# Kernel optimization log

Hardware: AMD Instinct MI355X
Metric: run time of the kernel (lower is better)

## Reference

```python
import jax, jax.numpy as jnp
import numpy as np


def setup_inputs() -> dict:
    key = jax.random.key(0)
    k1, k2, k3, k4, k5, k6 = jax.random.split(key, 6)
    B, S, V, E, H = 64, 128, 50257, 1024, 1024
    scale_ih = 1.0 / np.sqrt(H)
    return {
        "question_tokens": jax.random.randint(k1, (B, S), 0, V, dtype=jnp.int64),
        "emb_weights": jax.random.normal(k2, (V, E), dtype=jnp.float32),
        "w_ih": jax.random.normal(k3, (3 * H, E), dtype=jnp.float32) * scale_ih,
        "w_hh": jax.random.normal(k4, (3 * H, H), dtype=jnp.float32) * scale_ih,
        "b_ih": jax.random.normal(k5, (3 * H,), dtype=jnp.float32) * scale_ih,
        "b_hh": jax.random.normal(k6, (3 * H,), dtype=jnp.float32) * scale_ih,
    }


def _gru_last_hidden(tokens, emb_weights, w_ih, w_hh, b_ih, b_hh):
    # tokens: [B, S]; torch module transposes to seq-first, equivalent here.
    H = w_hh.shape[1]
    x = emb_weights[tokens]                                  # [B, S, E]
    # Precompute input projections for all timesteps (hoisted out of recurrence).
    x_proj = jnp.einsum("bse,ge->sbg", x, w_ih) + b_ih      # [S, B, 3H]

    def step(h, xp):
        # PyTorch GRU gate order: r, z, n
        hp = h @ w_hh.T + b_hh                               # [B, 3H]
        xr, xz, xn = xp[:, :H], xp[:, H:2 * H], xp[:, 2 * H:]
        hr, hz, hn = hp[:, :H], hp[:, H:2 * H], hp[:, 2 * H:]
        r = jax.nn.sigmoid(xr + hr)
        z = jax.nn.sigmoid(xz + hz)
        n = jnp.tanh(xn + r * hn)
        h_new = (1.0 - z) * n + z * h
        return h_new, None

    h0 = jnp.zeros((tokens.shape[0], H), dtype=emb_weights.dtype)
    hT, _ = jax.lax.scan(step, h0, x_proj)
    return hT                                                # [B, H]


def reference(question_tokens, emb_weights, w_ih, w_hh, b_ih, b_hh):
    return _gru_last_hidden(question_tokens, emb_weights, w_ih, w_hh, b_ih, b_hh)
```

## Files before the change

kernel.cpp:

```cpp
#include <hip/hip_runtime.h>
#include <hip/hip_bf16.h>
#include <math.h>

#define GRU_B 64
#define GRU_S 128
#define GRU_E 1024
#define GRU_H 1024
#define GRU_G 3072

typedef _Float16 half8 __attribute__((ext_vector_type(8)));
typedef _Float16 half4v __attribute__((ext_vector_type(4)));
typedef float floatx4 __attribute__((ext_vector_type(4)));

__device__ __forceinline__ half8 cvt_h8(float4 a, float4 b) {
    half8 r;
    r[0] = (_Float16)a.x; r[1] = (_Float16)a.y;
    r[2] = (_Float16)a.z; r[3] = (_Float16)a.w;
    r[4] = (_Float16)b.x; r[5] = (_Float16)b.y;
    r[6] = (_Float16)b.z; r[7] = (_Float16)b.w;
    return r;
}

__global__ __launch_bounds__(256) void xproj_mfma(
    const int* __restrict__ tokens,
    const float* __restrict__ emb,
    const float* __restrict__ w_ih,
    const float* __restrict__ b_ih,
    _Float16* __restrict__ xproj)
{
    __shared__ __attribute__((aligned(16))) _Float16 Al[128 * 32];
    __shared__ __attribute__((aligned(16))) _Float16 Bl[128 * 32];
    __shared__ int toks[128];

    const int t  = threadIdx.x;
    const int m0 = blockIdx.x * 128;
    const int n0 = blockIdx.y * 128;

    if (t < 128) {
        int m = m0 + t;
        toks[t] = tokens[(m & 63) * GRU_S + (m >> 6)];
    }

    const int wid = t >> 6;
    const int l   = t & 63;
    const int wm  = (wid >> 1) * 64;
    const int wn  = (wid & 1) * 64;

    const int sr   = t >> 1;
    const int skw  = (sr >> 1) & 3;
    const int gb   = (t & 1) * 2;

    const int fr   = l & 15;
    const int ag   = l >> 4;
    const int skey = (fr >> 1) & 3;
    const int gfr  = (ag ^ skey) * 16;

    char* ab = reinterpret_cast<char*>(Al);
    char* bb = reinterpret_cast<char*>(Bl);

    floatx4 acc[4][4];
#pragma unroll
    for (int i = 0; i < 4; ++i)
#pragma unroll
        for (int j = 0; j < 4; ++j)
            acc[i][j] = (floatx4){0.f, 0.f, 0.f, 0.f};

    for (int k0 = 0; k0 < GRU_E; k0 += 32) {
        __syncthreads();
        {
            const float4* asrc = reinterpret_cast<const float4*>(
                emb + (size_t)toks[sr] * GRU_E + k0 + (t & 1) * 16);
            const float4* bsrc = reinterpret_cast<const float4*>(
                w_ih + (size_t)(n0 + sr) * GRU_E + k0 + (t & 1) * 16);
            float4 a0 = asrc[0], a1 = asrc[1], a2 = asrc[2], a3 = asrc[3];
            float4 b0 = bsrc[0], b1 = bsrc[1], b2 = bsrc[2], b3 = bsrc[3];
            *reinterpret_cast<half8*>(ab + sr * 64 + ((gb + 0) ^ skw) * 16) = cvt_h8(a0, a1);
            *reinterpret_cast<half8*>(ab + sr * 64 + ((gb + 1) ^ skw) * 16) = cvt_h8(a2, a3);
            *reinterpret_cast<half8*>(bb + sr * 64 + ((gb + 0) ^ skw) * 16) = cvt_h8(b0, b1);
            *reinterpret_cast<half8*>(bb + sr * 64 + ((gb + 1) ^ skw) * 16) = cvt_h8(b2, b3);
        }
        __syncthreads();

        half8 a4[4], b4[4];
#pragma unroll
        for (int mi = 0; mi < 4; ++mi)
            a4[mi] = *reinterpret_cast<const half8*>(ab + (wm + mi * 16 + fr) * 64 + gfr);
#pragma unroll
        for (int ni = 0; ni < 4; ++ni)
            b4[ni] = *reinterpret_cast<const half8*>(bb + (wn + ni * 16 + fr) * 64 + gfr);
#pragma unroll
        for (int mi = 0; mi < 4; ++mi)
#pragma unroll
            for (int ni = 0; ni < 4; ++ni)
                acc[mi][ni] = __builtin_amdgcn_mfma_f32_16x16x32_f16(
                    a4[mi], b4[ni], acc[mi][ni], 0, 0, 0);
    }

    const int cr = (l >> 4) * 4;
    const int cc = l & 15;
#pragma unroll
    for (int ni = 0; ni < 4; ++ni) {
        int n = n0 + wn + ni * 16 + cc;
        float bias = b_ih[n];
#pragma unroll
        for (int mi = 0; mi < 4; ++mi) {
#pragma unroll
            for (int q = 0; q < 4; ++q) {
                int m = m0 + wm + mi * 16 + cr + q;
                xproj[(size_t)m * GRU_G + n] = (_Float16)(acc[mi][ni][q] + bias);
            }
        }
    }
}

__global__ __launch_bounds__(256) void gru_persist(
    const _Float16* __restrict__ xproj,
    const float* __restrict__ w_hh,
    const float* __restrict__ b_hh,
    _Float16* __restrict__ ring,
    float* __restrict__ out,
    int* __restrict__ flags)
{
    __shared__ __attribute__((aligned(16))) _Float16 wlds[48 * 1024];

    __builtin_amdgcn_fence(__ATOMIC_ACQUIRE, "agent");

    const int t   = threadIdx.x;
    const int jb  = blockIdx.x;
    const int l   = t & 63;
    const int wid = t >> 6;
    const int m0  = wid * 16;

    const size_t BUFE = (size_t)GRU_B * GRU_H;
    const size_t BUFQ = BUFE / 4;

    {
        char* wbp = reinterpret_cast<char*>(wlds);
        for (int r = 0; r < 48; ++r) {
            int grow = (r >> 4) * GRU_H + jb * 16 + (r & 15);
            float4 v = reinterpret_cast<const float4*>(
                w_hh + (size_t)grow * GRU_H)[t];
            half4v hv;
            hv.x = (_Float16)v.x; hv.y = (_Float16)v.y;
            hv.z = (_Float16)v.z; hv.w = (_Float16)v.w;
            int g = (t >> 1) ^ (r & 7);
            *reinterpret_cast<half4v*>(wbp + r * 2048 + g * 16 + (t & 1) * 8) = hv;
        }
    }

    {
        unsigned long long* z =
            reinterpret_cast<unsigned long long*>(ring) + 127 * BUFQ;
        int i0 = jb * 256 + t;
        (void)__hip_atomic_exchange(z + i0, 0ULL, __ATOMIC_RELAXED,
                                    __HIP_MEMORY_SCOPE_AGENT);
    }

    const int jl   = l & 15;
    const int qrow = (l >> 4) * 4;
    const int j    = jb * 16 + jl;
    const float bhr = b_hh[j];
    const float bhz = b_hh[GRU_H + j];
    const float bhn = b_hh[2 * GRU_H + j];

    const int arow  = m0 + (l & 15);
    const int akoff = (l >> 4) * 8;
    const int sk    = jl & 7;
    const char* wb  = reinterpret_cast<const char*>(wlds);
    const int bbase0 = (0 * 16 + jl) * 2048;
    const int bbase1 = (1 * 16 + jl) * 2048;
    const int bbase2 = (2 * 16 + jl) * 2048;

    const int colq   = (jb * 16 + jl) >> 2;
    const bool leader = ((l & 3) == 0);

    float hp[4] = {0.f, 0.f, 0.f, 0.f};
    float xr[4], xz[4], xnn[4];

    __syncthreads();
    if (t == 0)
        __hip_atomic_store(flags + jb, 1, __ATOMIC_RELAXED,
                           __HIP_MEMORY_SCOPE_AGENT);

#pragma unroll
    for (int q = 0; q < 4; ++q) {
        const _Float16* row = xproj + (size_t)(m0 + qrow + q) * GRU_G;
        xr[q]  = (float)row[j];
        xz[q]  = (float)row[GRU_H + j];
        xnn[q] = (float)row[2 * GRU_H + j];
    }

    for (int s = 0; s < GRU_S; ++s) {
        if (wid == 0) {
            const int tgt = s + 1;
            while (true) {
                int f = __hip_atomic_load(flags + l, __ATOMIC_RELAXED,
                                          __HIP_MEMORY_SCOPE_AGENT);
                if (__all(f >= tgt)) break;
                __builtin_amdgcn_s_sleep(1);
            }
        }
        __syncthreads();
        __builtin_amdgcn_sched_barrier(0);
        asm volatile("" ::: "memory");

        const _Float16* hbuf = ring + (size_t)(127 - s) * BUFE;
        const _Float16* aptr = hbuf + (size_t)arow * GRU_H + akoff;

        floatx4 acc0 = {0.f, 0.f, 0.f, 0.f};
        floatx4 acc1 = {0.f, 0.f, 0.f, 0.f};
        floatx4 acc2 = {0.f, 0.f, 0.f, 0.f};

#pragma unroll 8
        for (int kc = 0; kc < 32; ++kc) {
            half8 a = *reinterpret_cast<const half8*>(aptr + kc * 32);
            int g = (kc * 4 + (l >> 4)) ^ sk;
            half8 b0 = *reinterpret_cast<const half8*>(wb + bbase0 + g * 16);
            half8 b1 = *reinterpret_cast<const half8*>(wb + bbase1 + g * 16);
            half8 b2 = *reinterpret_cast<const half8*>(wb + bbase2 + g * 16);
            acc0 = __builtin_amdgcn_mfma_f32_16x16x32_f16(a, b0, acc0, 0, 0, 0);
            acc1 = __builtin_amdgcn_mfma_f32_16x16x32_f16(a, b1, acc1, 0, 0, 0);
            acc2 = __builtin_amdgcn_mfma_f32_16x16x32_f16(a, b2, acc2, 0, 0, 0);
        }

        const bool last = (s == GRU_S - 1);

        unsigned int dw[4];
#pragma unroll
        for (int q = 0; q < 4; ++q) {
            float r  = 1.f / (1.f + __expf(-(xr[q] + acc0[q] + bhr)));
            float zg = 1.f / (1.f + __expf(-(xz[q] + acc1[q] + bhz)));
            float pre = xnn[q] + r * (acc2[q] + bhn);
            pre = fminf(fmaxf(pre, -15.f), 15.f);
            float e2 = __expf(2.f * pre);
            float ng = (e2 - 1.f) / (e2 + 1.f);
            float h  = (1.f - zg) * ng + zg * hp[q];
            hp[q] = h;
            unsigned int hu = (unsigned int)__builtin_bit_cast(
                unsigned short, (_Float16)h);
            unsigned int ot = (unsigned int)__shfl_xor((int)hu, 1);
            dw[q] = hu | (ot << 16);
        }

        if (!last) {
            unsigned long long* wbuf =
                reinterpret_cast<unsigned long long*>(ring)
                + (size_t)(126 - s) * BUFQ;
#pragma unroll
            for (int q = 0; q < 4; ++q) {
                unsigned int hi = (unsigned int)__shfl_xor((int)dw[q], 2);
                if (leader) {
                    unsigned long long qw =
                        (unsigned long long)dw[q] |
                        ((unsigned long long)hi << 32);
                    (void)__hip_atomic_exchange(
                        wbuf + (size_t)(m0 + qrow + q) * 256 + colq, qw,
                        __ATOMIC_RELAXED, __HIP_MEMORY_SCOPE_AGENT);
                }
            }

            __syncthreads();
            if (t == 0)
                __hip_atomic_store(flags + jb, s + 2, __ATOMIC_RELAXED,
                                   __HIP_MEMORY_SCOPE_AGENT);
            asm volatile("" ::: "memory");

            const _Float16* xpS = xproj + (size_t)(s + 1) * (GRU_B * GRU_G);
#pragma unroll
            for (int q = 0; q < 4; ++q) {
                const _Float16* row = xpS + (size_t)(m0 + qrow + q) * GRU_G;
                xr[q]  = (float)row[j];
                xz[q]  = (float)row[GRU_H + j];
                xnn[q] = (float)row[2 * GRU_H + j];
            }
        }
    }

#pragma unroll
    for (int q = 0; q < 4; ++q)
        out[(size_t)(m0 + qrow + q) * GRU_H + j] = hp[q];
}

extern "C" void kernel_launch(void* const* d_in, const int* in_sizes, int n_in,
                              void* d_out, int out_size, void* d_ws, size_t ws_size,
                              hipStream_t stream) {
    const int*   tokens = (const int*)  d_in[0];
    const float* emb    = (const float*)d_in[1];
    const float* w_ih   = (const float*)d_in[2];
    const float* w_hh   = (const float*)d_in[3];
    const float* b_ih   = (const float*)d_in[4];
    const float* b_hh   = (const float*)d_in[5];
    float* out = (float*)d_out;

    _Float16* xproj16 = (_Float16*)d_ws;
    _Float16* ring    = xproj16 + (size_t)GRU_S * GRU_B * GRU_G;
    int*      flags   = (int*)(ring + 128 * (size_t)GRU_B * GRU_H);

    hipMemsetAsync(flags, 0, 64 * sizeof(int), stream);

    {
        dim3 grid(GRU_B * GRU_S / 128, GRU_G / 128);
        xproj_mfma<<<grid, 256, 0, stream>>>(tokens, emb, w_ih, b_ih, xproj16);
    }

    {
        const _Float16* xp_a = xproj16;
        const float* whh_a = w_hh;
        const float* bhh_a = b_hh;
        _Float16* ring_a = ring;
        float* out_a = out;
        int* flags_a = flags;
        void* args[] = { (void*)&xp_a, (void*)&whh_a, (void*)&bhh_a,
                         (void*)&ring_a, (void*)&out_a, (void*)&flags_a };
        hipLaunchCooperativeKernel((void*)gru_persist, dim3(64), dim3(256),
                                   args, 0, stream);
    }
}
```

Baseline: 880.8 us.

## Fuse input projection into persistent GRU kernel with producer blocks and counters

Result: faster. 857.1 us (-2.7%).

```diff
diff --git a/kernel.cpp b/kernel.cpp
--- a/kernel.cpp
+++ b/kernel.cpp
@@ -7,6 +7,9 @@
 #define GRU_E 1024
 #define GRU_H 1024
 #define GRU_G 3072
+
+#define XP_TILES 1536
+#define NPROD    192
 
 typedef _Float16 half8 __attribute__((ext_vector_type(8)));
 typedef _Float16 half4v __attribute__((ext_vector_type(4)));
@@ -21,115 +24,139 @@
     return r;
 }
 
-__global__ __launch_bounds__(256) void xproj_mfma(
+__global__ __launch_bounds__(256) void gru_fused(
     const int* __restrict__ tokens,
     const float* __restrict__ emb,
     const float* __restrict__ w_ih,
     const float* __restrict__ b_ih,
-    _Float16* __restrict__ xproj)
-{
-    __shared__ __attribute__((aligned(16))) _Float16 Al[128 * 32];
-    __shared__ __attribute__((aligned(16))) _Float16 Bl[128 * 32];
-    __shared__ int toks[128];
-
-    const int t  = threadIdx.x;
-    const int m0 = blockIdx.x * 128;
-    const int n0 = blockIdx.y * 128;
-
-    if (t < 128) {
-        int m = m0 + t;
-        toks[t] = tokens[(m & 63) * GRU_S + (m >> 6)];
-    }
-
-    const int wid = t >> 6;
-    const int l   = t & 63;
-    const int wm  = (wid >> 1) * 64;
-    const int wn  = (wid & 1) * 64;
-
-    const int sr   = t >> 1;
-    const int skw  = (sr >> 1) & 3;
-    const int gb   = (t & 1) * 2;
-
-    const int fr   = l & 15;
-    const int ag   = l >> 4;
-    const int skey = (fr >> 1) & 3;
-    const int gfr  = (ag ^ skey) * 16;
-
-    char* ab = reinterpret_cast<char*>(Al);
-    char* bb = reinterpret_cast<char*>(Bl);
-
-    floatx4 acc[4][4];
-#pragma unroll
-    for (int i = 0; i < 4; ++i)
-#pragma unroll
-        for (int j = 0; j < 4; ++j)
-            acc[i][j] = (floatx4){0.f, 0.f, 0.f, 0.f};
-
-    for (int k0 = 0; k0 < GRU_E; k0 += 32) {
-        __syncthreads();
-        {
-            const float4* asrc = reinterpret_cast<const float4*>(
-                emb + (size_t)toks[sr] * GRU_E + k0 + (t & 1) * 16);
-            const float4* bsrc = reinterpret_cast<const float4*>(
-                w_ih + (size_t)(n0 + sr) * GRU_E + k0 + (t & 1) * 16);
-            float4 a0 = asrc[0], a1 = asrc[1], a2 = asrc[2], a3 = asrc[3];
-            float4 b0 = bsrc[0], b1 = bsrc[1], b2 = bsrc[2], b3 = bsrc[3];
-            *reinterpret_cast<half8*>(ab + sr * 64 + ((gb + 0) ^ skw) * 16) = cvt_h8(a0, a1);
-            *reinterpret_cast<half8*>(ab + sr * 64 + ((gb + 1) ^ skw) * 16) = cvt_h8(a2, a3);
-            *reinterpret_cast<half8*>(bb + sr * 64 + ((gb + 0) ^ skw) * 16) = cvt_h8(b0, b1);
-            *reinterpret_cast<half8*>(bb + sr * 64 + ((gb + 1) ^ skw) * 16) = cvt_h8(b2, b3);
-        }
-        __syncthreads();
-
-        half8 a4[4], b4[4];
-#pragma unroll
-        for (int mi = 0; mi < 4; ++mi)
-            a4[mi] = *reinterpret_cast<const half8*>(ab + (wm + mi * 16 + fr) * 64 + gfr);
-#pragma unroll
-        for (int ni = 0; ni < 4; ++ni)
-            b4[ni] = *reinterpret_cast<const half8*>(bb + (wn + ni * 16 + fr) * 64 + gfr);
-#pragma unroll
-        for (int mi = 0; mi < 4; ++mi)
-#pragma unroll
-            for (int ni = 0; ni < 4; ++ni)
-                acc[mi][ni] = __builtin_amdgcn_mfma_f32_16x16x32_f16(
-                    a4[mi], b4[ni], acc[mi][ni], 0, 0, 0);
-    }
-
-    const int cr = (l >> 4) * 4;
-    const int cc = l & 15;
-#pragma unroll
-    for (int ni = 0; ni < 4; ++ni) {
-        int n = n0 + wn + ni * 16 + cc;
-        float bias = b_ih[n];
-#pragma unroll
-        for (int mi = 0; mi < 4; ++mi) {
-#pragma unroll
-            for (int q = 0; q < 4; ++q) {
-                int m = m0 + wm + mi * 16 + cr + q;
-                xproj[(size_t)m * GRU_G + n] = (_Float16)(acc[mi][ni][q] + bias);
-            }
-        }
-    }
-}
-
-__global__ __launch_bounds__(256) void gru_persist(
-    const _Float16* __restrict__ xproj,
+    _Float16* __restrict__ xproj,
     const float* __restrict__ w_hh,
     const float* __restrict__ b_hh,
     _Float16* __restrict__ ring,
     float* __restrict__ out,
-    int* __restrict__ flags)
+    int* __restrict__ flags,
+    int* __restrict__ xpcnt)
 {
-    __shared__ __attribute__((aligned(16))) _Float16 wlds[48 * 1024];
+    __shared__ __attribute__((aligned(16))) char sh[96 * 1024];
 
     __builtin_amdgcn_fence(__ATOMIC_ACQUIRE, "agent");
 
+    const int bid = blockIdx.x;
     const int t   = threadIdx.x;
-    const int jb  = blockIdx.x;
     const int l   = t & 63;
     const int wid = t >> 6;
-    const int m0  = wid * 16;
+
+    if (bid >= 64) {
+        _Float16* Al = reinterpret_cast<_Float16*>(sh);
+        _Float16* Bl = Al + 128 * 32;
+        int* toks    = reinterpret_cast<int*>(Bl + 128 * 32);
+
+        const int wm   = (wid >> 1) * 64;
+        const int wn   = (wid & 1) * 64;
+        const int sr   = t >> 1;
+        const int skw  = (sr >> 1) & 3;
+        const int gb   = (t & 1) * 2;
+        const int fr   = l & 15;
+        const int ag   = l >> 4;
+        const int skey = (fr >> 1) & 3;
+        const int gfr  = (ag ^ skey) * 16;
+        const int cr   = (l >> 4) * 4;
+        const int cc   = l & 15;
+        const bool leader = ((l & 3) == 0);
+
+        char* ab = reinterpret_cast<char*>(Al);
+        char* bb = reinterpret_cast<char*>(Bl);
+        unsigned long long* xp64 = reinterpret_cast<unsigned long long*>(xproj);
+
+        for (int T = bid - 64; T < XP_TILES; T += NPROD) {
+            const int sp = T / 24;
+            const int nt = T % 24;
+            const int m0 = sp * 128;
+            const int n0 = nt * 128;
+
+            if (t < 128) {
+                int m = m0 + t;
+                toks[t] = tokens[(m & 63) * GRU_S + (m >> 6)];
+            }
+
+            floatx4 acc[4][4];
+#pragma unroll
+            for (int i = 0; i < 4; ++i)
+#pragma unroll
+                for (int jj = 0; jj < 4; ++jj)
+                    acc[i][jj] = (floatx4){0.f, 0.f, 0.f, 0.f};
+
+            for (int k0 = 0; k0 < GRU_E; k0 += 32) {
+                __syncthreads();
+                {
+                    const float4* asrc = reinterpret_cast<const float4*>(
+                        emb + (size_t)toks[sr] * GRU_E + k0 + (t & 1) * 16);
+                    const float4* bsrc = reinterpret_cast<const float4*>(
+                        w_ih + (size_t)(n0 + sr) * GRU_E + k0 + (t & 1) * 16);
+                    float4 a0 = asrc[0], a1 = asrc[1], a2 = asrc[2], a3 = asrc[3];
+                    float4 b0 = bsrc[0], b1 = bsrc[1], b2 = bsrc[2], b3 = bsrc[3];
+                    *reinterpret_cast<half8*>(ab + sr * 64 + ((gb + 0) ^ skw) * 16) = cvt_h8(a0, a1);
+                    *reinterpret_cast<half8*>(ab + sr * 64 + ((gb + 1) ^ skw) * 16) = cvt_h8(a2, a3);
+                    *reinterpret_cast<half8*>(bb + sr * 64 + ((gb + 0) ^ skw) * 16) = cvt_h8(b0, b1);
+                    *reinterpret_cast<half8*>(bb + sr * 64 + ((gb + 1) ^ skw) * 16) = cvt_h8(b2, b3);
+                }
+                __syncthreads();
+
+                half8 a4[4], b4[4];
+#pragma unroll
+                for (int mi = 0; mi < 4; ++mi)
+                    a4[mi] = *reinterpret_cast<const half8*>(ab + (wm + mi * 16 + fr) * 64 + gfr);
+#pragma unroll
+                for (int ni = 0; ni < 4; ++ni)
+                    b4[ni] = *reinterpret_cast<const half8*>(bb + (wn + ni * 16 + fr) * 64 + gfr);
+#pragma unroll
+                for (int mi = 0; mi < 4; ++mi)
+#pragma unroll
+                    for (int ni = 0; ni < 4; ++ni)
+                        acc[mi][ni] = __builtin_amdgcn_mfma_f32_16x16x32_f16(
+                            a4[mi], b4[ni], acc[mi][ni], 0, 0, 0);
+            }
+
+#pragma unroll
+            for (int ni = 0; ni < 4; ++ni) {
+                const int n = n0 + wn + ni * 16 + cc;
+                const float bias = b_ih[n];
+                const int nb4 = (n0 + wn + ni * 16 + (cc & ~3)) >> 2;
+#pragma unroll
+                for (int mi = 0; mi < 4; ++mi) {
+#pragma unroll
+                    for (int q = 0; q < 4; ++q) {
+                        const int m = m0 + wm + mi * 16 + cr + q;
+                        float v = acc[mi][ni][q] + bias;
+                        unsigned int hu = (unsigned int)__builtin_bit_cast(
+                            unsigned short, (_Float16)v);
+                        unsigned int ot = (unsigned int)__shfl_xor((int)hu, 1);
+                        unsigned int dwq = hu | (ot << 16);
+                        unsigned int hi = (unsigned int)__shfl_xor((int)dwq, 2);
+                        if (leader) {
+                            unsigned long long qw =
+                                (unsigned long long)dwq |
+                                ((unsigned long long)hi << 32);
+                            (void)__hip_atomic_exchange(
+                                xp64 + (size_t)m * (GRU_G / 4) + nb4, qw,
+                                __ATOMIC_RELAXED, __HIP_MEMORY_SCOPE_AGENT);
+                        }
+                    }
+                }
+            }
+
+            __syncthreads();
+            if (t == 0)
+                __hip_atomic_fetch_add(xpcnt + sp, 1, __ATOMIC_RELAXED,
+                                       __HIP_MEMORY_SCOPE_AGENT);
+        }
+        return;
+    }
+
+    _Float16* wlds = reinterpret_cast<_Float16*>(sh);
+
+    const int jb = bid;
+    const int m0 = wid * 16;
 
     const size_t BUFE = (size_t)GRU_B * GRU_H;
     const size_t BUFQ = BUFE / 4;
@@ -182,6 +209,10 @@
         __hip_atomic_store(flags + jb, 1, __ATOMIC_RELAXED,
                            __HIP_MEMORY_SCOPE_AGENT);
 
+    while (__hip_atomic_load(xpcnt + 0, __ATOMIC_RELAXED,
+                             __HIP_MEMORY_SCOPE_AGENT) < 24)
+        __builtin_amdgcn_s_sleep(2);
+    asm volatile("" ::: "memory");
 #pragma unroll
     for (int q = 0; q < 4; ++q) {
         const _Float16* row = xproj + (size_t)(m0 + qrow + q) * GRU_G;
@@ -265,6 +296,11 @@
                                    __HIP_MEMORY_SCOPE_AGENT);
             asm volatile("" ::: "memory");
 
+            const int spn = (s + 1) >> 1;
+            while (__hip_atomic_load(xpcnt + spn, __ATOMIC_RELAXED,
+                                     __HIP_MEMORY_SCOPE_AGENT) < 24)
+                __builtin_amdgcn_s_sleep(2);
+            asm volatile("" ::: "memory");
             const _Float16* xpS = xproj + (size_t)(s + 1) * (GRU_B * GRU_G);
 #pragma unroll
             for (int q = 0; q < 4; ++q) {
@@ -295,24 +331,27 @@
     _Float16* xproj16 = (_Float16*)d_ws;
     _Float16* ring    = xproj16 + (size_t)GRU_S * GRU_B * GRU_G;
     int*      flags   = (int*)(ring + 128 * (size_t)GRU_B * GRU_H);
-
-    hipMemsetAsync(flags, 0, 64 * sizeof(int), stream);
+    int*      xpcnt   = flags + 64;
+
+    hipMemsetAsync(flags, 0, 128 * sizeof(int), stream);
 
     {
-        dim3 grid(GRU_B * GRU_S / 128, GRU_G / 128);
-        xproj_mfma<<<grid, 256, 0, stream>>>(tokens, emb, w_ih, b_ih, xproj16);
-    }
-
-    {
-        const _Float16* xp_a = xproj16;
+        const int* tok_a = tokens;
+        const float* emb_a = emb;
+        const float* wih_a = w_ih;
+        const float* bih_a = b_ih;
+        _Float16* xp_a = xproj16;
         const float* whh_a = w_hh;
         const float* bhh_a = b_hh;
         _Float16* ring_a = ring;
         float* out_a = out;
         int* flags_a = flags;
-        void* args[] = { (void*)&xp_a, (void*)&whh_a, (void*)&bhh_a,
-                         (void*)&ring_a, (void*)&out_a, (void*)&flags_a };
-        hipLaunchCooperativeKernel((void*)gru_persist, dim3(64), dim3(256),
+        int* xpcnt_a = xpcnt;
+        void* args[] = { (void*)&tok_a, (void*)&emb_a, (void*)&wih_a,
+                         (void*)&bih_a, (void*)&xp_a, (void*)&whh_a,
+                         (void*)&bhh_a, (void*)&ring_a, (void*)&out_a,
+                         (void*)&flags_a, (void*)&xpcnt_a };
+        hipLaunchCooperativeKernel((void*)gru_fused, dim3(256), dim3(256),
                                    args, 0, stream);
     }
 }
```
